# Kernel optimization log

Measured on AMD Instinct MI355X. Metric: run time of the kernel, lower is better.

The kernel has to match this reference:

```python
import jax, jax.numpy as jnp
import numpy as np

D_MODEL = 1024
NUM_HEADS = 16
D_K = D_MODEL // NUM_HEADS


def setup_inputs() -> dict:
    key = jax.random.key(0)
    ks = jax.random.split(key, 12)
    B, S = 1, 4096
    s = 1.0 / np.sqrt(D_MODEL)
    inp = {
        'query': jax.random.normal(ks[0], (B, S, D_MODEL), jnp.float32),
        'key': jax.random.normal(ks[1], (B, S, D_MODEL), jnp.float32),
        'value': jax.random.normal(ks[2], (B, S, D_MODEL), jnp.float32),
        'W_q': jax.random.normal(ks[3], (D_MODEL, D_MODEL), jnp.float32) * s,
        'b_q': jnp.zeros((D_MODEL,), jnp.float32),
        'W_k': jax.random.normal(ks[4], (D_MODEL, D_MODEL), jnp.float32) * s,
        'b_k': jnp.zeros((D_MODEL,), jnp.float32),
        'W_v': jax.random.normal(ks[5], (D_MODEL, D_MODEL), jnp.float32) * s,
        'b_v': jnp.zeros((D_MODEL,), jnp.float32),
        'W_o': jax.random.normal(ks[6], (D_MODEL, D_MODEL), jnp.float32) * s,
        'b_o': jnp.zeros((D_MODEL,), jnp.float32),
    }
    return inp


def reference(query, key, value, W_q, b_q, W_k, b_k, W_v, b_v, W_o, b_o):
    B, S, _ = query.shape
    # torch nn.Linear: y = x @ W.T + b
    Q = query @ W_q.T + b_q
    K = key @ W_k.T + b_k
    V = value @ W_v.T + b_v
    # (B, S, H, d_k) -> (B, H, S, d_k)
    Q = Q.reshape(B, S, NUM_HEADS, D_K).transpose(0, 2, 1, 3)
    K = K.reshape(B, S, NUM_HEADS, D_K).transpose(0, 2, 1, 3)
    V = V.reshape(B, S, NUM_HEADS, D_K).transpose(0, 2, 1, 3)
    scale = 1.0 / jnp.sqrt(jnp.asarray(D_K, Q.dtype))
    qk = jnp.einsum('bhqd,bhkd->bhqk', Q, K) * scale  # [B,H,S,S]
    attn = jax.nn.softmax(qk, axis=-1)
    out = jnp.einsum('bhqk,bhkd->bhqd', attn, V)
    out = out.transpose(0, 2, 1, 3).reshape(B, S, D_MODEL)
    return out @ W_o.T + b_o
```

## Files before the change

### kernel.cpp

```cpp
#include <hip/hip_runtime.h>
#include <cstdint>
#include <cstddef>

typedef __bf16 bf16_t;
typedef _Float16 f16_t;
typedef __attribute__((ext_vector_type(8))) __bf16 bf16x8;
typedef __attribute__((ext_vector_type(4))) __bf16 bf16x4;
typedef __attribute__((ext_vector_type(2))) __bf16 bf16x2;
typedef __attribute__((ext_vector_type(8))) _Float16 f16x8;
typedef __attribute__((ext_vector_type(2))) _Float16 f16x2;
typedef __attribute__((ext_vector_type(4))) float floatx4;
typedef __attribute__((ext_vector_type(2))) float floatx2;
typedef __attribute__((ext_vector_type(16))) float floatx16;
typedef __attribute__((ext_vector_type(2))) int i32x2;

#define S_LEN 4096
#define DM 1024
#define NH 16
#define DKH 64
#define NSPLIT 4
#define KT_PER (S_LEN / 64 / NSPLIT)

#define QSCALE 0.1803368801111601f

__device__ __forceinline__ void async_b128(void* lds, const void* g) {
    __builtin_amdgcn_global_load_lds(
        (__attribute__((address_space(1))) void*)(uintptr_t)g,
        (__attribute__((address_space(3))) void*)lds,
        16, 0, 0);
}

__device__ __forceinline__ void fence_all() { __builtin_amdgcn_s_waitcnt(0); }

__device__ __forceinline__ floatx4 mfma16(bf16x8 a, bf16x8 b, floatx4 c) {
    return __builtin_amdgcn_mfma_f32_16x16x32_bf16(a, b, c, 0, 0, 0);
}
__device__ __forceinline__ floatx16 mfma32(bf16x8 a, bf16x8 b, floatx16 c) {
    return __builtin_amdgcn_mfma_f32_32x32x16_bf16(a, b, c, 0, 0, 0);
}
__device__ __forceinline__ int f2i(float x) { return __builtin_bit_cast(int, x); }
__device__ __forceinline__ float i2f(int x) { return __builtin_bit_cast(float, x); }
__device__ __forceinline__ int p2i(bf16x2 x) { return __builtin_bit_cast(int, x); }

__global__ __launch_bounds__(256) void convert_all_kernel(
    const float* __restrict__ q, const float* __restrict__ k,
    const float* __restrict__ v, const float* __restrict__ wqf,
    const float* __restrict__ wkf, const float* __restrict__ wvf,
    const float* __restrict__ wof, bf16_t* __restrict__ dst_in,
    bf16_t* __restrict__ dst_w) {
    const size_t i = ((size_t)blockIdx.x * 256 + threadIdx.x) * 4;
    const float* s;
    bf16_t* d;
    size_t off;
    if (i < 12582912) {
        const int r = (int)(i >> 22);
        s = (r == 0) ? q : (r == 1) ? k : v;
        off = i & 4194303;
        d = dst_in + (size_t)r * 4194304 + off;
    } else {
        const size_t j = i - 12582912;
        const int r = (int)(j >> 20);
        s = (r == 0) ? wqf : (r == 1) ? wkf : (r == 2) ? wvf : wof;
        off = j & 1048575;
        d = dst_w + (size_t)r * 1048576 + off;
    }
    const floatx4 val = *(const floatx4*)(s + off);
    bf16x4 o;
    o[0] = (bf16_t)val[0]; o[1] = (bf16_t)val[1];
    o[2] = (bf16_t)val[2]; o[3] = (bf16_t)val[3];
    *(bf16x4*)d = o;
}

template <int BN, typename OutT>
__device__ __forceinline__ void gemm_bt_body(const bf16_t* __restrict__ A,
                                             const bf16_t* __restrict__ B,
                                             const float* __restrict__ bias,
                                             OutT* __restrict__ C, float oscale) {
    constexpr int K = 1024, N = 1024;
    constexpr int NT = BN / 32;
    __shared__ bf16_t As[128 * 32];
    __shared__ bf16_t Bs[BN * 32];
    const int tid = threadIdx.x;
    const int wid = tid >> 6, lane = tid & 63;
    const int quad = lane >> 4, l16 = lane & 15;
    const int m0 = blockIdx.y * 128, n0 = blockIdx.x * BN;
    const int wm = (wid & 1) * 64, wn = (wid >> 1) * (BN / 2);

    floatx4 acc[4][NT] = {};

    for (int k0 = 0; k0 < K; k0 += 32) {
        __syncthreads();
#pragma unroll
        for (int i = 0; i < 2; ++i) {
            const int c = (i << 8) + tid;
            const int row = c >> 2;
            const int ko = (c & 3) << 3;
            const int lb = ((i << 8) + (wid << 6)) << 3;
            async_b128(&As[lb], A + (size_t)(m0 + row) * K + k0 + ko);
        }
#pragma unroll
        for (int i = 0; i < BN / 64; ++i) {
            const int c = (i << 8) + tid;
            const int row = c >> 2;
            const int ko = (c & 3) << 3;
            const int lb = ((i << 8) + (wid << 6)) << 3;
            async_b128(&Bs[lb], B + (size_t)(n0 + row) * K + k0 + ko);
        }
        fence_all();
        __syncthreads();

        bf16x8 af[4], bfr[NT];
#pragma unroll
        for (int t = 0; t < 4; ++t)
            af[t] = *(const bf16x8*)&As[(wm + t * 16 + l16) * 32 + quad * 8];
#pragma unroll
        for (int t = 0; t < NT; ++t)
            bfr[t] = *(const bf16x8*)&Bs[(wn + t * 16 + l16) * 32 + quad * 8];
#pragma unroll
        for (int mt = 0; mt < 4; ++mt)
#pragma unroll
            for (int nt = 0; nt < NT; ++nt)
                acc[mt][nt] = mfma16(af[mt], bfr[nt], acc[mt][nt]);
    }

#pragma unroll
    for (int mt = 0; mt < 4; ++mt)
#pragma unroll
        for (int nt = 0; nt < NT; ++nt) {
            const int col = n0 + wn + nt * 16 + l16;
            const float bv = bias[col];
#pragma unroll
            for (int r = 0; r < 4; ++r) {
                const int row = m0 + wm + mt * 16 + quad * 4 + r;
                C[(size_t)row * N + col] = (OutT)((acc[mt][nt][r] + bv) * oscale);
            }
        }
}

__global__ __launch_bounds__(256) void gemm_qkv_kernel(
    const bf16_t* __restrict__ qx, const bf16_t* __restrict__ kx,
    const bf16_t* __restrict__ vx, const bf16_t* __restrict__ wq,
    const bf16_t* __restrict__ wk, const bf16_t* __restrict__ wv,
    const float* __restrict__ bq, const float* __restrict__ bk,
    const float* __restrict__ bv, bf16_t* __restrict__ Qp,
    bf16_t* __restrict__ Kp, bf16_t* __restrict__ Vp) {
    const int z = blockIdx.z;
    const bf16_t* A = (z == 0) ? qx : (z == 1) ? kx : vx;
    const bf16_t* B = (z == 0) ? wq : (z == 1) ? wk : wv;
    const float* bias = (z == 0) ? bq : (z == 1) ? bk : bv;
    bf16_t* C = (z == 0) ? Qp : (z == 1) ? Kp : Vp;
    gemm_bt_body<128, bf16_t>(A, B, bias, C, (z == 0) ? QSCALE : 1.0f);
}

__global__ __launch_bounds__(256) void gemm_out_kernel(
    const bf16_t* __restrict__ AO, const bf16_t* __restrict__ wo,
    const float* __restrict__ bo, float* __restrict__ out) {
    gemm_bt_body<64, float>(AO, wo, bo, out, 1.0f);
}

__global__ __launch_bounds__(256) void transpose_kernel(
    const bf16_t* __restrict__ in, bf16_t* __restrict__ out) {
    __shared__ bf16_t tile[64][65];
    const int tx = threadIdx.x & 63;
    const int ty = threadIdx.x >> 6;
    const int c0 = blockIdx.x * 64;
    const int r0 = blockIdx.y * 64;
#pragma unroll
    for (int i = 0; i < 16; ++i) {
        const int r = ty + i * 4;
        tile[r][tx] = in[(size_t)(r0 + r) * DM + c0 + tx];
    }
    __syncthreads();
#pragma unroll
    for (int i = 0; i < 16; ++i) {
        const int c = ty + i * 4;
        out[(size_t)(c0 + c) * S_LEN + r0 + tx] = tile[tx][c];
    }
}

__global__ __launch_bounds__(256, 2) void flash_kernel(
    const bf16_t* __restrict__ Q, const bf16_t* __restrict__ K,
    const bf16_t* __restrict__ Vt, f16_t* __restrict__ Opart,
    float* __restrict__ Lpart) {
    __shared__ bf16_t smem[16384];
    bf16_t* Ks = smem;
    bf16_t* Vs = smem + 8192;

    const int tid = threadIdx.x;
    const int wave = tid >> 6, lane = tid & 63;
    const int h32 = lane >> 5, c = lane & 31;
    const int head = blockIdx.y;
    const int sp = blockIdx.z;
    const int qbase = blockIdx.x * 256 + wave * 64;
    const int kv0 = sp * (S_LEN / NSPLIT);

    bf16x8 Qf[2][4];
#pragma unroll
    for (int nt = 0; nt < 2; ++nt)
#pragma unroll
        for (int s = 0; s < 4; ++s)
            Qf[nt][s] = *(const bf16x8*)(Q + (size_t)(qbase + nt * 32 + c) * DM +
                                         head * DKH + s * 16 + h32 * 8);

    floatx16 oa[2][2] = {};
    floatx2 la2[2][2] = {};

    const bf16_t* kptr = K + (size_t)(kv0 + lane) * DM + head * DKH + wave * 16;
    const bf16_t* vptr = Vt + (size_t)(head * DKH + lane) * S_LEN + kv0 + wave * 16;
    bf16_t* ksl = Ks + wave * 1024;
    bf16_t* vsl = Vs + wave * 1024;

    async_b128(ksl, kptr);       async_b128(ksl + 512, kptr + 8);
    async_b128(vsl, vptr);       async_b128(vsl + 512, vptr + 8);
    kptr += 64 * DM; vptr += 64;

    for (int kt = 0; kt < KT_PER; ++kt) {
        const int buf = kt & 1;
        fence_all();
        __syncthreads();
        if (kt + 1 < KT_PER) {
            bf16_t* kd = ksl + (buf ^ 1) * 4096;
            bf16_t* vd = vsl + (buf ^ 1) * 4096;
            async_b128(kd, kptr);     async_b128(kd + 512, kptr + 8);
            async_b128(vd, vptr);     async_b128(vd + 512, vptr + 8);
            kptr += 64 * DM; vptr += 64;
        }

        bf16x8 Kf[2][4];
#pragma unroll
        for (int mt = 0; mt < 2; ++mt)
#pragma unroll
            for (int s = 0; s < 4; ++s)
                Kf[mt][s] = *(const bf16x8*)&Ks[buf * 4096 + ((2 * s + h32) * 64 + mt * 32 + c) * 8];

        floatx16 sc[2][2];
#pragma unroll
        for (int mt = 0; mt < 2; ++mt)
#pragma unroll
            for (int nt = 0; nt < 2; ++nt)
#pragma unroll
                for (int j = 0; j < 16; ++j)
                    sc[mt][nt][j] = -3.0f;

#pragma unroll
        for (int s = 0; s < 4; ++s)
#pragma unroll
            for (int mt = 0; mt < 2; ++mt)
#pragma unroll
                for (int nt = 0; nt < 2; ++nt)
                    sc[mt][nt] = mfma32(Kf[mt][s], Qf[nt][s], sc[mt][nt]);

        bf16x8 Vf[2][4];
#pragma unroll
        for (int dt = 0; dt < 2; ++dt)
#pragma unroll
            for (int s = 0; s < 4; ++s)
                Vf[dt][s] = *(const bf16x8*)&Vs[buf * 4096 + ((2 * s + h32) * 64 + dt * 32 + c) * 8];

#pragma unroll
        for (int nt = 0; nt < 2; ++nt) {
            int pk[2][8];
#pragma unroll
            for (int mt = 0; mt < 2; ++mt)
#pragma unroll
                for (int rr = 0; rr < 8; ++rr) {
                    const float p0 = __builtin_amdgcn_exp2f(sc[mt][nt][2 * rr]);
                    const float p1 = __builtin_amdgcn_exp2f(sc[mt][nt][2 * rr + 1]);
                    la2[nt][rr & 1] += floatx2{p0, p1};
                    bf16x2 w; w[0] = (bf16_t)p0; w[1] = (bf16_t)p1;
                    pk[mt][rr] = p2i(w);
                }
#pragma unroll
            for (int s = 0; s < 4; ++s) {
                const int a = s >> 1, b4 = (s & 1) * 4;
                const i32x2 r02 = __builtin_amdgcn_permlane32_swap(
                    pk[a][b4 + 0], pk[a][b4 + 2], false, false);
                const i32x2 r13 = __builtin_amdgcn_permlane32_swap(
                    pk[a][b4 + 1], pk[a][b4 + 3], false, false);
                union { bf16x8 v; int d[4]; } P;
                P.d[0] = r02[0];
                P.d[1] = r13[0];
                P.d[2] = r02[1];
                P.d[3] = r13[1];
                oa[0][nt] = mfma32(Vf[0][s], P.v, oa[0][nt]);
                oa[1][nt] = mfma32(Vf[1][s], P.v, oa[1][nt]);
            }
        }
    }

#pragma unroll
    for (int nt = 0; nt < 2; ++nt) {
        float t = la2[nt][0][0] + la2[nt][0][1] + la2[nt][1][0] + la2[nt][1][1];
        t += i2f(__shfl_xor(f2i(t), 32));
        if (h32 == 0)
            Lpart[(size_t)(sp * NH + head) * S_LEN + qbase + nt * 32 + c] = t;
    }

    fence_all();
    __syncthreads();
    f16_t* ot = (f16_t*)smem + wave * (32 * 72);
#pragma unroll
    for (int nt = 0; nt < 2; ++nt) {
#pragma unroll
        for (int dt = 0; dt < 2; ++dt)
#pragma unroll
            for (int rr = 0; rr < 8; ++rr) {
                const int d0 = dt * 32 + ((2 * rr) & 3) + 8 * (rr >> 1) + 4 * h32;
                f16x2 w;
                w[0] = (f16_t)oa[dt][nt][2 * rr];
                w[1] = (f16_t)oa[dt][nt][2 * rr + 1];
                *(f16x2*)&ot[c * 72 + d0] = w;
            }
        fence_all();
        __syncthreads();
        const int r = lane & 31;
#pragma unroll
        for (int j = 0; j < 4; ++j) {
            const f16x8 v = *(const f16x8*)&ot[r * 72 + h32 * 32 + j * 8];
            *(f16x8*)(Opart + ((size_t)sp * S_LEN + qbase + nt * 32 + r) * DM +
                      head * DKH + h32 * 32 + j * 8) = v;
        }
        fence_all();
        __syncthreads();
    }
}

__global__ __launch_bounds__(256) void reduce_kernel(
    const f16_t* __restrict__ Op, const float* __restrict__ Lp,
    bf16_t* __restrict__ AO) {
    const size_t f = ((size_t)blockIdx.x * 256 + threadIdx.x) * 8;
    const int q = (int)(f >> 10);
    const int h = (int)((f & 1023) >> 6);
    float l = 0.f;
#pragma unroll
    for (int sp = 0; sp < NSPLIT; ++sp)
        l += Lp[(size_t)(sp * NH + h) * S_LEN + q];
    const float inv = 1.0f / l;
    float s[8] = {};
#pragma unroll
    for (int sp = 0; sp < NSPLIT; ++sp) {
        const f16x8 v = *(const f16x8*)(Op + (size_t)sp * (S_LEN * DM) + f);
#pragma unroll
        for (int j = 0; j < 8; ++j) s[j] += (float)v[j];
    }
    bf16x8 o;
#pragma unroll
    for (int j = 0; j < 8; ++j) o[j] = (bf16_t)(s[j] * inv);
    *(bf16x8*)(AO + f) = o;
}

extern "C" void kernel_launch(void* const* d_in, const int* in_sizes, int n_in,
                              void* d_out, int out_size, void* d_ws, size_t ws_size,
                              hipStream_t stream) {
    const float* q  = (const float*)d_in[0];
    const float* k  = (const float*)d_in[1];
    const float* v  = (const float*)d_in[2];
    const float* Wq = (const float*)d_in[3];
    const float* bq = (const float*)d_in[4];
    const float* Wk = (const float*)d_in[5];
    const float* bk = (const float*)d_in[6];
    const float* Wv = (const float*)d_in[7];
    const float* bv = (const float*)d_in[8];
    const float* Wo = (const float*)d_in[9];
    const float* bo = (const float*)d_in[10];
    float* out = (float*)d_out;

    bf16_t* ws = (bf16_t*)d_ws;
    bf16_t* qx = ws;
    bf16_t* kx = qx + 4194304;
    bf16_t* vx = kx + 4194304;
    bf16_t* Vp = vx + 4194304;
    f16_t*  Opart = (f16_t*)ws;
    bf16_t* wq = Vp + 4194304;
    bf16_t* wk = wq + 1048576;
    bf16_t* wv = wk + 1048576;
    bf16_t* wo = wv + 1048576;
    bf16_t* Qp = wo + 1048576;
    bf16_t* Kp = Qp + 4194304;
    bf16_t* Vt = Kp + 4194304;
    bf16_t* AO = Vt + 4194304;
    float*  Lpart = (float*)(AO + 4194304);

    convert_all_kernel<<<dim3(16384), 256, 0, stream>>>(q, k, v, Wq, Wk, Wv, Wo,
                                                        qx, wq);
    gemm_qkv_kernel<<<dim3(8, 32, 3), 256, 0, stream>>>(qx, kx, vx, wq, wk, wv,
                                                        bq, bk, bv, Qp, Kp, Vp);
    transpose_kernel<<<dim3(16, 64), 256, 0, stream>>>(Vp, Vt);
    flash_kernel<<<dim3(16, 16, NSPLIT), 256, 0, stream>>>(Qp, Kp, Vt, Opart, Lpart);
    reduce_kernel<<<dim3(2048), 256, 0, stream>>>(Opart, Lpart, AO);
    gemm_out_kernel<<<dim3(16, 32), 256, 0, stream>>>(AO, wo, bo, out);
    (void)in_sizes; (void)n_in; (void)out_size; (void)ws_size;
}
```

Baseline: 258.6 us.

## Fuse activation fp32-to-bf16 conversion into QKV GEMM, halve split-K, add MFMA priority

Result: slower. 277.3 us (+7.2%).

```diff
diff --git a/kernel.cpp b/kernel.cpp
--- a/kernel.cpp
+++ b/kernel.cpp
@@ -18,7 +18,7 @@
 #define DM 1024
 #define NH 16
 #define DKH 64
-#define NSPLIT 4
+#define NSPLIT 2
 #define KT_PER (S_LEN / 64 / NSPLIT)
 
 #define QSCALE 0.1803368801111601f
@@ -42,42 +42,29 @@
 __device__ __forceinline__ float i2f(int x) { return __builtin_bit_cast(float, x); }
 __device__ __forceinline__ int p2i(bf16x2 x) { return __builtin_bit_cast(int, x); }
 
-__global__ __launch_bounds__(256) void convert_all_kernel(
-    const float* __restrict__ q, const float* __restrict__ k,
-    const float* __restrict__ v, const float* __restrict__ wqf,
-    const float* __restrict__ wkf, const float* __restrict__ wvf,
-    const float* __restrict__ wof, bf16_t* __restrict__ dst_in,
+__global__ __launch_bounds__(256) void convert_w_kernel(
+    const float* __restrict__ wqf, const float* __restrict__ wkf,
+    const float* __restrict__ wvf, const float* __restrict__ wof,
     bf16_t* __restrict__ dst_w) {
     const size_t i = ((size_t)blockIdx.x * 256 + threadIdx.x) * 4;
-    const float* s;
-    bf16_t* d;
-    size_t off;
-    if (i < 12582912) {
-        const int r = (int)(i >> 22);
-        s = (r == 0) ? q : (r == 1) ? k : v;
-        off = i & 4194303;
-        d = dst_in + (size_t)r * 4194304 + off;
-    } else {
-        const size_t j = i - 12582912;
-        const int r = (int)(j >> 20);
-        s = (r == 0) ? wqf : (r == 1) ? wkf : (r == 2) ? wvf : wof;
-        off = j & 1048575;
-        d = dst_w + (size_t)r * 1048576 + off;
-    }
+    const int r = (int)(i >> 20);
+    const float* s = (r == 0) ? wqf : (r == 1) ? wkf : (r == 2) ? wvf : wof;
+    const size_t off = i & 1048575;
     const floatx4 val = *(const floatx4*)(s + off);
     bf16x4 o;
     o[0] = (bf16_t)val[0]; o[1] = (bf16_t)val[1];
     o[2] = (bf16_t)val[2]; o[3] = (bf16_t)val[3];
-    *(bf16x4*)d = o;
-}
-
-template <int BN, typename OutT>
-__device__ __forceinline__ void gemm_bt_body(const bf16_t* __restrict__ A,
+    *(bf16x4*)(dst_w + (size_t)r * 1048576 + off) = o;
+}
+
+template <int BN, typename OutT, typename AT>
+__device__ __forceinline__ void gemm_bt_body(const AT* __restrict__ A,
                                              const bf16_t* __restrict__ B,
                                              const float* __restrict__ bias,
                                              OutT* __restrict__ C, float oscale) {
     constexpr int K = 1024, N = 1024;
     constexpr int NT = BN / 32;
+    constexpr bool CVTA = (sizeof(AT) == 4);
     __shared__ bf16_t As[128 * 32];
     __shared__ bf16_t Bs[BN * 32];
     const int tid = threadIdx.x;
@@ -91,14 +78,6 @@
     for (int k0 = 0; k0 < K; k0 += 32) {
         __syncthreads();
 #pragma unroll
-        for (int i = 0; i < 2; ++i) {
-            const int c = (i << 8) + tid;
-            const int row = c >> 2;
-            const int ko = (c & 3) << 3;
-            const int lb = ((i << 8) + (wid << 6)) << 3;
-            async_b128(&As[lb], A + (size_t)(m0 + row) * K + k0 + ko);
-        }
-#pragma unroll
         for (int i = 0; i < BN / 64; ++i) {
             const int c = (i << 8) + tid;
             const int row = c >> 2;
@@ -106,6 +85,31 @@
             const int lb = ((i << 8) + (wid << 6)) << 3;
             async_b128(&Bs[lb], B + (size_t)(n0 + row) * K + k0 + ko);
         }
+        if constexpr (CVTA) {
+            const int row = tid >> 1, ko = (tid & 1) << 4;
+            const float* ap = A + (size_t)(m0 + row) * K + k0 + ko;
+            const floatx4 f0 = *(const floatx4*)(ap);
+            const floatx4 f1 = *(const floatx4*)(ap + 4);
+            const floatx4 f2 = *(const floatx4*)(ap + 8);
+            const floatx4 f3 = *(const floatx4*)(ap + 12);
+            bf16x8 b0, b1;
+#pragma unroll
+            for (int j = 0; j < 4; ++j) {
+                b0[j] = (bf16_t)f0[j]; b0[4 + j] = (bf16_t)f1[j];
+                b1[j] = (bf16_t)f2[j]; b1[4 + j] = (bf16_t)f3[j];
+            }
+            *(bf16x8*)&As[row * 32 + ko] = b0;
+            *(bf16x8*)&As[row * 32 + ko + 8] = b1;
+        } else {
+#pragma unroll
+            for (int i = 0; i < 2; ++i) {
+                const int c = (i << 8) + tid;
+                const int row = c >> 2;
+                const int ko = (c & 3) << 3;
+                const int lb = ((i << 8) + (wid << 6)) << 3;
+                async_b128(&As[lb], (const bf16_t*)A + (size_t)(m0 + row) * K + k0 + ko);
+            }
+        }
         fence_all();
         __syncthreads();
 
@@ -138,24 +142,24 @@
 }
 
 __global__ __launch_bounds__(256) void gemm_qkv_kernel(
-    const bf16_t* __restrict__ qx, const bf16_t* __restrict__ kx,
-    const bf16_t* __restrict__ vx, const bf16_t* __restrict__ wq,
+    const float* __restrict__ q, const float* __restrict__ k,
+    const float* __restrict__ v, const bf16_t* __restrict__ wq,
     const bf16_t* __restrict__ wk, const bf16_t* __restrict__ wv,
     const float* __restrict__ bq, const float* __restrict__ bk,
     const float* __restrict__ bv, bf16_t* __restrict__ Qp,
     bf16_t* __restrict__ Kp, bf16_t* __restrict__ Vp) {
     const int z = blockIdx.z;
-    const bf16_t* A = (z == 0) ? qx : (z == 1) ? kx : vx;
+    const float* A = (z == 0) ? q : (z == 1) ? k : v;
     const bf16_t* B = (z == 0) ? wq : (z == 1) ? wk : wv;
     const float* bias = (z == 0) ? bq : (z == 1) ? bk : bv;
     bf16_t* C = (z == 0) ? Qp : (z == 1) ? Kp : Vp;
-    gemm_bt_body<128, bf16_t>(A, B, bias, C, (z == 0) ? QSCALE : 1.0f);
+    gemm_bt_body<128, bf16_t, float>(A, B, bias, C, (z == 0) ? QSCALE : 1.0f);
 }
 
 __global__ __launch_bounds__(256) void gemm_out_kernel(
     const bf16_t* __restrict__ AO, const bf16_t* __restrict__ wo,
     const float* __restrict__ bo, float* __restrict__ out) {
-    gemm_bt_body<64, float>(AO, wo, bo, out, 1.0f);
+    gemm_bt_body<64, float, bf16_t>(AO, wo, bo, out, 1.0f);
 }
 
 __global__ __launch_bounds__(256) void transpose_kernel(
@@ -242,6 +246,7 @@
                 for (int j = 0; j < 16; ++j)
                     sc[mt][nt][j] = -3.0f;
 
+        __builtin_amdgcn_s_setprio(1);
 #pragma unroll
         for (int s = 0; s < 4; ++s)
 #pragma unroll
@@ -249,6 +254,7 @@
 #pragma unroll
                 for (int nt = 0; nt < 2; ++nt)
                     sc[mt][nt] = mfma32(Kf[mt][s], Qf[nt][s], sc[mt][nt]);
+        __builtin_amdgcn_s_setprio(0);
 
         bf16x8 Vf[2][4];
 #pragma unroll
@@ -270,6 +276,7 @@
                     bf16x2 w; w[0] = (bf16_t)p0; w[1] = (bf16_t)p1;
                     pk[mt][rr] = p2i(w);
                 }
+            __builtin_amdgcn_s_setprio(1);
 #pragma unroll
             for (int s = 0; s < 4; ++s) {
                 const int a = s >> 1, b4 = (s & 1) * 4;
@@ -285,6 +292,7 @@
                 oa[0][nt] = mfma32(Vf[0][s], P.v, oa[0][nt]);
                 oa[1][nt] = mfma32(Vf[1][s], P.v, oa[1][nt]);
             }
+            __builtin_amdgcn_s_setprio(0);
         }
     }
 
@@ -366,11 +374,7 @@
     float* out = (float*)d_out;
 
     bf16_t* ws = (bf16_t*)d_ws;
-    bf16_t* qx = ws;
-    bf16_t* kx = qx + 4194304;
-    bf16_t* vx = kx + 4194304;
-    bf16_t* Vp = vx + 4194304;
-    f16_t*  Opart = (f16_t*)ws;
+    bf16_t* Vp = ws;
     bf16_t* wq = Vp + 4194304;
     bf16_t* wk = wq + 1048576;
     bf16_t* wv = wk + 1048576;
@@ -379,11 +383,11 @@
     bf16_t* Kp = Qp + 4194304;
     bf16_t* Vt = Kp + 4194304;
     bf16_t* AO = Vt + 4194304;
-    float*  Lpart = (float*)(AO + 4194304);
-
-    convert_all_kernel<<<dim3(16384), 256, 0, stream>>>(q, k, v, Wq, Wk, Wv, Wo,
-                                                        qx, wq);
-    gemm_qkv_kernel<<<dim3(8, 32, 3), 256, 0, stream>>>(qx, kx, vx, wq, wk, wv,
+    f16_t*  Opart = (f16_t*)(AO + 4194304);
+    float*  Lpart = (float*)(AO + 4194304 + (size_t)NSPLIT * 4194304);
+
+    convert_w_kernel<<<dim3(4096), 256, 0, stream>>>(Wq, Wk, Wv, Wo, wq);
+    gemm_qkv_kernel<<<dim3(8, 32, 3), 256, 0, stream>>>(q, k, v, wq, wk, wv,
                                                         bq, bk, bv, Qp, Kp, Vp);
     transpose_kernel<<<dim3(16, 64), 256, 0, stream>>>(Vp, Vt);
     flash_kernel<<<dim3(16, 16, NSPLIT), 256, 0, stream>>>(Qp, Kp, Vt, Opart, Lpart);
```
